# Performance work log

Measured on AMD Instinct MI355X. Metric: run time of the kernel, lower is better.

## Reference

```python
import jax, jax.numpy as jnp
import numpy as np

# architecture constants (from __init__)
F = 34          # input frequency bands
K = 7           # rrf_kernel_size
S = 3           # rrf_stride
F_DOWN = (F - K) // S + 1   # 10
C = 64          # hidden_channels
H = F_DOWN * C  # 640
T_MAX = 9       # max_delay (dilated kernel size of Dcls1d)
PAD = (T_MAX - 1) // 2
MS_KS = 200     # minisobel (freq-dependent high-pass exponential) kernel size
W_MS = 0.75
BN_EPS = 1e-5


def setup_inputs() -> dict:
    key = jax.random.key(0)
    ks = jax.random.split(key, 10)
    B, T = 32, 1000
    def g(k, sh, scale):
        return jax.random.normal(k, sh, jnp.float32) * scale
    x = jax.random.normal(ks[0], (B, 1, F, T), jnp.float32)
    # minisobel params: per-frequency EMA coefficient a in (0,1), mixing weight w
    a_vals = jax.random.uniform(ks[1], (F,), jnp.float32, 0.05, 0.5)
    w_vals = jnp.full((F,), W_MS, jnp.float32)
    # DCLS params: one weight + one continuous delay position per synapse
    dcls_w = g(ks[2], (H, 2 * K), 1.0 / np.sqrt(2 * K * T_MAX))
    dcls_p = jax.random.uniform(ks[3], (H, 2 * K), jnp.float32, 0.0, T_MAX - 1.0)
    dcls_b = jnp.zeros((H,), jnp.float32)
    bn_gamma = jnp.ones((C,), jnp.float32)
    bn_beta = jnp.zeros((C,), jnp.float32)
    s = 1.0 / np.sqrt(H)
    W_ih = g(ks[4], (3 * H, H), s)
    W_hh = g(ks[5], (3 * H, H), s)
    b_ih = g(ks[6], (3 * H,), s)
    b_hh = g(ks[7], (3 * H,), s)
    fc_w = g(ks[8], (1, H), s)
    fc_b = jnp.zeros((1,), jnp.float32)
    return dict(x=x, a_vals=a_vals, w_vals=w_vals, dcls_w=dcls_w, dcls_p=dcls_p,
                dcls_b=dcls_b, bn_gamma=bn_gamma, bn_beta=bn_beta,
                W_ih=W_ih, W_hh=W_hh, b_ih=b_ih, b_hh=b_hh, fc_w=fc_w, fc_b=fc_b)


def reference(x, a_vals, w_vals, dcls_w, dcls_p, dcls_b, bn_gamma, bn_beta,
              W_ih, W_hh, b_ih, b_hh, fc_w, fc_b):
    B, T = x.shape[0], x.shape[-1]
    xf = x[:, 0]  # [B,F,T]

    # --- minisobel: per-frequency causal exponential low-pass, high-pass residual,
    #     on/off rectified channels -> [B,2,F,T]
    t_idx = jnp.arange(MS_KS, dtype=x.dtype)
    ema = a_vals[:, None] * (1.0 - a_vals[:, None]) ** t_idx[None, :]  # [F,200]
    ema = ema[:, ::-1][:, None, :]  # flip so correlation = causal convolution
    low = jax.lax.conv_general_dilated(xf, ema, (1,), [(MS_KS - 1, 0)],
                                       dimension_numbers=('NCH', 'OIH', 'NCH'),
                                       feature_group_count=F)
    hp = xf - w_vals[None, :, None] * low
    x2 = jnp.stack([jax.nn.relu(hp), jax.nn.relu(-hp)], axis=1)  # [B,2,F,T]

    # --- unfold over frequency (kernel (K,T), stride (S,1)) + reshape
    #     -> [B, F_down*2*K, T], channels grouped per output frequency band
    rows = jnp.arange(F_DOWN)[:, None] * S + jnp.arange(K)[None, :]  # [F_down,K]
    u = x2[:, :, rows, :]                      # [B,2,F_down,K,T]
    u = u.transpose(0, 2, 1, 3, 4).reshape(B, F_DOWN * 2 * K, T)

    # --- Dcls1d: build interpolated kernel (triangle interpolation of one weight
    #     at a learnable fractional delay), grouped 'same' conv over time
    p = jnp.clip(dcls_p, 0.0, T_MAX - 1.0)     # [H,2K]
    tt = jnp.arange(T_MAX, dtype=x.dtype)
    dk = dcls_w[:, :, None] * jax.nn.relu(1.0 - jnp.abs(tt[None, None, :] - p[:, :, None]))  # [H,2K,T_max]
    y = jax.lax.conv_general_dilated(u, dk, (1,), [(PAD, PAD)],
                                     dimension_numbers=('NCH', 'OIH', 'NCH'),
                                     feature_group_count=F_DOWN)
    y = y + dcls_b[None, :, None]              # [B,H,T]

    # --- [T,B,C,F_down], BatchNorm1d(C) over (T*B, F_down), sigmoid
    y = y.reshape(B, F_DOWN, C, T).transpose(3, 0, 2, 1)  # [T,B,C,F_down]
    mean = y.mean(axis=(0, 1, 3), keepdims=True)
    var = y.var(axis=(0, 1, 3), keepdims=True)
    y = (y - mean) * jax.lax.rsqrt(var + BN_EPS)
    y = jax.nn.sigmoid(y * bn_gamma[None, None, :, None] + 0 + bn_beta[None, None, :, None]) if False else jax.nn.sigmoid(y * bn_gamma[None, None, :, None] + bn_beta[None, None, :, None])

    # --- GRU (torch gate order r,z,n), batch_first output of all hidden states
    seq = y.reshape(T, B, H)
    x_proj = seq @ W_ih.T + b_ih               # [T,B,3H]

    def step(h, xp):
        gh = h @ W_hh.T + b_hh
        xr, xz, xn = jnp.split(xp, 3, axis=-1)
        hr, hz, hn = jnp.split(gh, 3, axis=-1)
        r = jax.nn.sigmoid(xr + hr)
        z = jax.nn.sigmoid(xz + hz)
        n = jnp.tanh(xn + r * hn)
        h = (1.0 - z) * n + z * h
        return h, h

    h0 = jnp.zeros((B, H), x.dtype)
    _, hs = jax.lax.scan(step, h0, x_proj)     # [T,B,H]

    out = hs @ fc_w.T + fc_b                   # [T,B,1]
    return out[..., 0].T                       # [B,T]
```

## Files before the change

### kernel.cpp

```cpp
#include <hip/hip_runtime.h>
#include <hip/hip_fp16.h>
#include <cstdint>

typedef float f4 __attribute__((ext_vector_type(4)));
typedef _Float16 h2v __attribute__((ext_vector_type(2)));
typedef _Float16 half8 __attribute__((ext_vector_type(8)));
typedef unsigned long long u64;


__global__ void k_dk(const float* __restrict__ dcls_w, const float* __restrict__ dcls_p,
                     float* __restrict__ dk) {
    int idx = blockIdx.x * 256 + threadIdx.x;
    if (idx >= 640 * 126) return;
    int h = idx / 126;
    int r = idx % 126;
    int i = r / 9;
    int tau = r % 9;
    float p = dcls_p[h * 14 + i];
    p = fminf(fmaxf(p, 0.f), 8.f);
    float tri = fmaxf(1.f - fabsf((float)tau - p), 0.f);
    dk[idx] = dcls_w[h * 14 + i] * tri;
}

__global__ void k_ema(const float* __restrict__ x, const float* __restrict__ a_vals,
                      const float* __restrict__ w_vals, float* __restrict__ hp) {
    __shared__ float xr[1024];
    int bf = blockIdx.x;
    int f = bf % 34;
    int tid = threadIdx.x;
    const float* xs = x + (size_t)bf * 1000;
    for (int i = tid; i < 1000; i += 256) xr[i] = xs[i];
    for (int i = 1000 + tid; i < 1024; i += 256) xr[i] = 0.f;
    __syncthreads();
    float a = a_vals[f], wv = w_vals[f];
    float om = 1.f - a;
    int t1 = tid, t2 = tid + 256, t3 = tid + 512, t4 = tid + 768;
    bool v4 = (t4 < 1000);
    float a0 = 0.f, a1 = 0.f, a2 = 0.f, a3 = 0.f;
    float coef = a;
    for (int k = 0; k < 200; ++k) {
        a0 += (k <= t1 ? xr[t1 - k] : 0.f) * coef;
        a1 += xr[t2 - k] * coef;
        a2 += xr[t3 - k] * coef;
        a3 += (v4 ? xr[t4 - k] : 0.f) * coef;
        coef *= om;
    }
    float* op = hp + (size_t)bf * 1000;
    op[t1] = xr[t1] - wv * a0;
    op[t2] = xr[t2] - wv * a1;
    op[t3] = xr[t3] - wv * a2;
    if (v4) op[t4] = xr[t4] - wv * a3;
}

__global__ void __launch_bounds__(256) k_conv(const float* __restrict__ hp,
                                              const float* __restrict__ dk,
                                              const float* __restrict__ dcls_b,
                                              float* __restrict__ ybcgt) {
    __shared__ float u[2 * 7 * 264];
    __shared__ float dks[64 * 126];
    int tid = threadIdx.x;
    int t0 = blockIdx.x * 256;
    int g = blockIdx.y;
    int b = blockIdx.z;
    for (int idx = tid; idx < 8064; idx += 256) dks[idx] = dk[g * 8064 + idx];
    for (int idx = tid; idx < 3696; idx += 256) {
        int pm = idx / 1848;
        int rem = idx % 1848;
        int kk = rem / 264;
        int tt = rem % 264;
        int tg = t0 - 4 + tt;
        float v = (tg >= 0 && tg < 1000) ? hp[((size_t)(b * 34 + g * 3 + kk)) * 1000 + tg] : 0.f;
        u[idx] = pm ? fmaxf(-v, 0.f) : fmaxf(v, 0.f);
    }
    __syncthreads();
    int tl = tid & 63;
    int cg4 = tid >> 6;
    float acc[16][4];
#pragma unroll
    for (int ci = 0; ci < 16; ++ci)
#pragma unroll
        for (int tq = 0; tq < 4; ++tq) acc[ci][tq] = 0.f;

    for (int i = 0; i < 14; ++i) {
#pragma unroll
        for (int tau = 0; tau < 9; ++tau) {
            const float* ub = u + i * 264 + tl + tau;
            float u0 = ub[0];
            float u1 = ub[64];
            float u2 = ub[128];
            float u3 = ub[192];
            const float* dp = dks + cg4 * 16 * 126 + i * 9 + tau;
#pragma unroll
            for (int ci = 0; ci < 16; ++ci) {
                float dv = dp[ci * 126];
                acc[ci][0] += u0 * dv;
                acc[ci][1] += u1 * dv;
                acc[ci][2] += u2 * dv;
                acc[ci][3] += u3 * dv;
            }
        }
    }
#pragma unroll
    for (int ci = 0; ci < 16; ++ci) {
        int c = cg4 * 16 + ci;
        float bias = dcls_b[g * 64 + c];
        size_t base = ((size_t)(b * 640 + c * 10 + g)) * 1000;
#pragma unroll
        for (int tq = 0; tq < 4; ++tq) {
            int t = t0 + tq * 64 + tl;
            if (t < 1000) ybcgt[base + t] = acc[ci][tq] + bias;
        }
    }
}

__global__ void k_bnstat(const float* __restrict__ ybcgt, float* __restrict__ bnsum) {
    int c = blockIdx.x / 10;
    int g = blockIdx.x % 10;
    int tid = threadIdx.x;
    float s = 0.f, q = 0.f;
    const float* base = ybcgt + ((size_t)(c * 10 + g)) * 1000;
    for (int b = 0; b < 32; ++b) {
        const float* p = base + (size_t)b * 640000;
        for (int t = tid; t < 1000; t += 256) {
            float v = p[t];
            s += v;
            q += v * v;
        }
    }
    for (int off = 1; off < 64; off <<= 1) {
        s += __shfl_xor(s, off);
        q += __shfl_xor(q, off);
    }
    __shared__ float rs[4], rq[4];
    if ((tid & 63) == 0) { rs[tid >> 6] = s; rq[tid >> 6] = q; }
    __syncthreads();
    if (tid == 0) {
        s = rs[0] + rs[1] + rs[2] + rs[3];
        q = rq[0] + rq[1] + rq[2] + rq[3];
        atomicAdd(&bnsum[c], s);
        atomicAdd(&bnsum[64 + c], q);
    }
}

__global__ void k_bnfin(const float* __restrict__ bnsum, const float* __restrict__ gamma,
                        const float* __restrict__ beta, float* __restrict__ bnp) {
    int c = threadIdx.x;
    const float inv_n = 1.f / 320000.f;
    float mean = bnsum[c] * inv_n;
    float var = bnsum[64 + c] * inv_n - mean * mean;
    float sc = gamma[c] * rsqrtf(var + 1e-5f);
    bnp[c] = sc;
    bnp[64 + c] = beta[c] - mean * sc;
}

__global__ void k_tr(const float* __restrict__ ybcgt, const float* __restrict__ bnp,
                     __half* __restrict__ seq) {
    __shared__ float tile[64 * 65];
    int tid = threadIdx.x;
    int tt0 = blockIdx.x * 64;
    int h0 = blockIdx.y * 64;
    int b = blockIdx.z;
    int tx = tid & 63;
    int ty = tid >> 6;
#pragma unroll
    for (int r = 0; r < 16; ++r) {
        int hh = r * 4 + ty;
        int t = tt0 + tx;
        float v = (t < 1000) ? ybcgt[((size_t)(b * 640 + h0 + hh)) * 1000 + t] : 0.f;
        int c = (h0 + hh) / 10;
        float sarg = bnp[c] * v + bnp[64 + c];
        tile[hh * 65 + tx] = 1.f / (1.f + __expf(-sarg));
    }
    __syncthreads();
#pragma unroll
    for (int r = 0; r < 16; ++r) {
        int t = tt0 + r * 4 + ty;
        if (t < 1000)
            seq[((size_t)t * 32 + b) * 640 + h0 + tx] = __float2half(tile[tx * 65 + r * 4 + ty]);
    }
}

__global__ void __launch_bounds__(256, 2) k_gemm(const __half* __restrict__ A,
                                                 const float* __restrict__ W,
                                                 const float* __restrict__ bih,
                                                 __half* __restrict__ C) {
    __shared__ __align__(16) _Float16 As[128 * 40];
    __shared__ __align__(16) _Float16 Bs[128 * 40];
    const int tid = threadIdx.x;
    const int n0 = blockIdx.x * 128;
    const int m0 = blockIdx.y * 128;
    const int lane = tid & 63;
    const int wid = tid >> 6;
    const int ml = lane & 15;
    const int kq = lane >> 4;
    const int wm = (wid & 1) * 64;
    const int wn = (wid >> 1) * 64;
    const int sr = tid >> 1;
    const int sc = (tid & 1) * 16;

    f4 acc[4][4];
#pragma unroll
    for (int mt = 0; mt < 4; ++mt)
#pragma unroll
        for (int nt = 0; nt < 4; ++nt) acc[mt][nt] = (f4){0.f, 0.f, 0.f, 0.f};

    const __half* Ag = A + (size_t)(m0 + sr) * 640 + sc;
    const float* Wg = W + (size_t)(n0 + sr) * 640 + sc;

    for (int s = 0; s < 20; ++s) {
        const int k0 = s * 32;
        half8 a0 = *(const half8*)(Ag + k0);
        half8 a1 = *(const half8*)(Ag + k0 + 8);
        float4 b0 = *(const float4*)(Wg + k0);
        float4 b1 = *(const float4*)(Wg + k0 + 4);
        float4 b2 = *(const float4*)(Wg + k0 + 8);
        float4 b3 = *(const float4*)(Wg + k0 + 12);
        __syncthreads();
        *(half8*)&As[sr * 40 + sc] = a0;
        *(half8*)&As[sr * 40 + sc + 8] = a1;
        half8 bh0 = {(_Float16)b0.x, (_Float16)b0.y, (_Float16)b0.z, (_Float16)b0.w,
                     (_Float16)b1.x, (_Float16)b1.y, (_Float16)b1.z, (_Float16)b1.w};
        half8 bh1 = {(_Float16)b2.x, (_Float16)b2.y, (_Float16)b2.z, (_Float16)b2.w,
                     (_Float16)b3.x, (_Float16)b3.y, (_Float16)b3.z, (_Float16)b3.w};
        *(half8*)&Bs[sr * 40 + sc] = bh0;
        *(half8*)&Bs[sr * 40 + sc + 8] = bh1;
        __syncthreads();
        half8 af[4], bf[4];
#pragma unroll
        for (int mt = 0; mt < 4; ++mt)
            af[mt] = *(const half8*)&As[(wm + mt * 16 + ml) * 40 + kq * 8];
#pragma unroll
        for (int nt = 0; nt < 4; ++nt)
            bf[nt] = *(const half8*)&Bs[(wn + nt * 16 + ml) * 40 + kq * 8];
#pragma unroll
        for (int mt = 0; mt < 4; ++mt)
#pragma unroll
            for (int nt = 0; nt < 4; ++nt)
                acc[mt][nt] = __builtin_amdgcn_mfma_f32_16x16x32_f16(af[mt], bf[nt],
                                                                     acc[mt][nt], 0, 0, 0);
    }
#pragma unroll
    for (int nt = 0; nt < 4; ++nt) {
        int n = n0 + wn + nt * 16 + ml;
        float bias = bih[n];
#pragma unroll
        for (int mt = 0; mt < 4; ++mt) {
            int mbase = m0 + wm + mt * 16 + kq * 4;
#pragma unroll
            for (int i = 0; i < 4; ++i)
                C[(size_t)(mbase + i) * 1920 + n] = __float2half(acc[mt][nt][i] + bias);
        }
    }
}

__global__ void __launch_bounds__(512, 1) k_gru(const __half* __restrict__ xp,
                                                const float* __restrict__ Whh,
                                                const float* __restrict__ bhh,
                                                const float* __restrict__ fcw,
                                                u64* __restrict__ slowb,
                                                u64* __restrict__ fastb,
                                                float* __restrict__ fcpart) {
    __shared__ __align__(16) h2v h_lds[16 * 324];
    __shared__ __align__(16) float red[4 * 33 * 4];
    __shared__ float fcred[2][4];

    const int tid = threadIdx.x;
    const int blk = blockIdx.x;
    const int grp = blk & 7;
    const int sl = blk >> 3;
    const int lane = tid & 63;
    const int wid = tid >> 6;

    u64* const sbase = slowb + (size_t)grp * 2560;
    u64* const fbase = fastb + (size_t)grp * 2560;

    const int gte = wid >> 1, jt = wid & 1;
    half8 afrag[20];
    if (wid < 6) {
        int m = lane & 15;
        int kq = lane >> 4;
        const float* wrow = Whh + (size_t)(gte * 640 + sl * 32 + jt * 16 + m) * 640;
#pragma unroll
        for (int s = 0; s < 20; ++s) {
            float4 w0 = *(const float4*)&wrow[s * 32 + kq * 8];
            float4 w1 = *(const float4*)&wrow[s * 32 + kq * 8 + 4];
            afrag[s] = (half8){(_Float16)w0.x, (_Float16)w0.y, (_Float16)w0.z, (_Float16)w0.w,
                               (_Float16)w1.x, (_Float16)w1.y, (_Float16)w1.z, (_Float16)w1.w};
        }
    }
    for (int i = tid; i < 16 * 324; i += 512) h_lds[i] = (h2v){(_Float16)0.f, (_Float16)0.f};

    const int e0 = tid, e1 = tid + 512;
    const bool has3 = (tid < 256);
    const int e2 = has3 ? tid + 1024 : tid;

    const int je = tid >> 2;
    const int be = tid & 3;
    float bh_r = 0.f, bh_z = 0.f, bh_n = 0.f, fw = 0.f, hold = 0.f;
    float xr = 0.f, xz = 0.f, xn = 0.f;
    if (tid < 128) {
        int jg = sl * 32 + je;
        bh_r = bhh[jg];
        bh_z = bhh[640 + jg];
        bh_n = bhh[1280 + jg];
        fw = fcw[jg];
        int bg = grp * 4 + be;
        const __half* xpt = xp + (size_t)bg * 1920;
        xr = __half2float(xpt[jg]);
        xz = __half2float(xpt[640 + jg]);
        xn = __half2float(xpt[1280 + jg]);
    }
    __syncthreads();

    for (int t = 0; t < 1000; ++t) {
        u64* const scur = sbase + (size_t)(t & 1) * 1280;
        u64* const snxt = sbase + (size_t)((t + 1) & 1) * 1280;
        u64* const fcur = fbase + (size_t)(t & 1) * 1280;
        u64* const fnxt = fbase + (size_t)((t + 1) & 1) * 1280;

        u64 v0 = 0, v1 = 0, v2 = 0;
        bool g0 = false, g1 = false, g2 = !has3;
        const unsigned tg = (unsigned)t;
        int round = 0;
        for (;;) {
            u64 f0, f1, f2;
            asm volatile(
                "global_load_dwordx2 %0, %3, off sc0\n\t"
                "global_load_dwordx2 %1, %4, off sc0\n\t"
                "global_load_dwordx2 %2, %5, off sc0\n\t"
                "s_waitcnt vmcnt(0)"
                : "=&v"(f0), "=&v"(f1), "=&v"(f2)
                : "v"(fcur + e0), "v"(fcur + e1), "v"(fcur + e2)
                : "memory");
            if (!g0 && (unsigned)(f0 >> 32) == tg) { v0 = f0; g0 = true; }
            if (!g1 && (unsigned)(f1 >> 32) == tg) { v1 = f1; g1 = true; }
            if (!g2 && (unsigned)(f2 >> 32) == tg) { v2 = f2; g2 = true; }
            if (g0 & g1 & g2) break;
            if ((round & 3) == 2) {
                if (!g0) {
                    u64 s0 = __hip_atomic_load(&scur[e0], __ATOMIC_RELAXED, __HIP_MEMORY_SCOPE_AGENT);
                    if ((unsigned)(s0 >> 32) == tg) { v0 = s0; g0 = true; }
                }
                if (!g1) {
                    u64 s1 = __hip_atomic_load(&scur[e1], __ATOMIC_RELAXED, __HIP_MEMORY_SCOPE_AGENT);
                    if ((unsigned)(s1 >> 32) == tg) { v1 = s1; g1 = true; }
                }
                if (!g2) {
                    u64 s2 = __hip_atomic_load(&scur[e2], __ATOMIC_RELAXED, __HIP_MEMORY_SCOPE_AGENT);
                    if ((unsigned)(s2 >> 32) == tg) { v2 = s2; g2 = true; }
                }
                if (g0 & g1 & g2) break;
            }
            __builtin_amdgcn_s_sleep(1);
            ++round;
        }
        {
            union { unsigned u; h2v h; } pk;
            pk.u = (unsigned)v0; h_lds[(e0 & 3) * 324 + (e0 >> 2)] = pk.h;
            pk.u = (unsigned)v1; h_lds[(e1 & 3) * 324 + (e1 >> 2)] = pk.h;
            if (has3) { pk.u = (unsigned)v2; h_lds[(e2 & 3) * 324 + (e2 >> 2)] = pk.h; }
        }
        __syncthreads();

        float nxr = 0.f, nxz = 0.f, nxn = 0.f;
        if (t + 1 < 1000 && tid < 128) {
            int jg = sl * 32 + je;
            int bg = grp * 4 + be;
            const __half* xpt = xp + ((size_t)(t + 1) * 32 + bg) * 1920;
            nxr = __half2float(xpt[jg]);
            nxz = __half2float(xpt[640 + jg]);
            nxn = __half2float(xpt[1280 + jg]);
        }

        if (wid < 6) {
            int bb = lane & 15;
            int kq = lane >> 4;
            const h2v* hb = &h_lds[bb * 324 + kq * 4];
            f4 acc = {0.f, 0.f, 0.f, 0.f};
#pragma unroll
            for (int s = 0; s < 20; ++s) {
                half8 bfrag = *(const half8*)&hb[s * 16];
                acc = __builtin_amdgcn_mfma_f32_16x16x32_f16(afrag[s], bfrag, acc, 0, 0, 0);
            }
            if (bb < 4) {
#pragma unroll
                for (int i = 0; i < 4; ++i)
                    red[(bb * 33 + jt * 16 + kq * 4 + i) * 4 + gte] = acc[i];
            }
        }
        __syncthreads();

        if (tid < 128) {
            f4 rv = *(const f4*)&red[(be * 33 + je) * 4];
            float hr = bh_r + rv.x;
            float hz = bh_z + rv.y;
            float hn = bh_n + rv.z;
            float r_ = 1.f / (1.f + __expf(-(xr + hr)));
            float z_ = 1.f / (1.f + __expf(-(xz + hz)));
            float pre = xn + r_ * hn;
            float e2v = __expf(-2.f * fabsf(pre));
            float tn = (1.f - e2v) / (1.f + e2v);
            float n_ = (pre >= 0.f) ? tn : -tn;
            float hnew = (1.f - z_) * n_ + z_ * hold;
            hold = hnew;
            float hpair = __shfl_xor(hnew, 4);
            if ((je & 1) == 0) {
                union { h2v h2; unsigned u; } cv;
                cv.h2.x = (_Float16)hnew;
                cv.h2.y = (_Float16)hpair;
                u64 val = (u64)cv.u | ((u64)(unsigned)(t + 1) << 32);
                size_t eo = (size_t)((sl * 16 + (je >> 1)) * 4 + be);
                u64* fp = fnxt + eo;
                asm volatile("global_store_dwordx2 %0, %1, off sc0" :: "v"(fp), "v"(val) : "memory");
                (void)__hip_atomic_exchange(snxt + eo, val,
                                            __ATOMIC_RELAXED, __HIP_MEMORY_SCOPE_AGENT);
            }
            float fv = hnew * fw;
            fv += __shfl_xor(fv, 4);
            fv += __shfl_xor(fv, 8);
            fv += __shfl_xor(fv, 16);
            fv += __shfl_xor(fv, 32);
            if (lane < 4) fcred[wid][lane] = fv;
        }
        xr = nxr; xz = nxz; xn = nxn;
        __syncthreads();
        if (tid < 4)
            fcpart[(size_t)blk * 4000 + t * 4 + tid] = fcred[0][tid] + fcred[1][tid];
    }
}

__global__ void k_fc(const float* __restrict__ fcpart, const float* __restrict__ fcb,
                     float* __restrict__ out) {
    int gid = blockIdx.x * 256 + threadIdx.x;
    int t = gid >> 5;
    int b = gid & 31;
    int g = b >> 2, bi = b & 3;
    float s = fcb[0];
    for (int sl = 0; sl < 20; ++sl)
        s += fcpart[(size_t)(g + 8 * sl) * 4000 + t * 4 + bi];
    out[(size_t)b * 1000 + t] = s;
}

extern "C" void kernel_launch(void* const* d_in, const int* in_sizes, int n_in,
                              void* d_out, int out_size, void* d_ws, size_t ws_size,
                              hipStream_t stream) {
    const float* x      = (const float*)d_in[0];
    const float* a_vals = (const float*)d_in[1];
    const float* w_vals = (const float*)d_in[2];
    const float* dcls_w = (const float*)d_in[3];
    const float* dcls_p = (const float*)d_in[4];
    const float* dcls_b = (const float*)d_in[5];
    const float* gamma  = (const float*)d_in[6];
    const float* beta   = (const float*)d_in[7];
    const float* W_ih   = (const float*)d_in[8];
    const float* W_hh   = (const float*)d_in[9];
    const float* b_ih   = (const float*)d_in[10];
    const float* b_hh   = (const float*)d_in[11];
    const float* fc_w   = (const float*)d_in[12];
    const float* fc_b   = (const float*)d_in[13];
    char* w = (char*)d_ws;

    __half* xpH    = (__half*)(w);
    float* ybcgt   = (float*)(w);
    __half* seqH   = (__half*)(w + 122880000);
    float* hp      = (float*)(w + 122880000);
    float* dk      = (float*)(w + 122880000 + 4352000);
    float* fcpart  = (float*)(w + 122880000);
    u64* fastb     = (u64*)(w + 125440000);
    u64* slowb     = (u64*)(w + 163840000);
    float* bnsum   = (float*)(w + 164003840);

    hipMemsetAsync(w + 163840000, 0, 166912, stream);

    k_dk<<<dim3(315), dim3(256), 0, stream>>>(dcls_w, dcls_p, dk);
    k_ema<<<dim3(1088), dim3(256), 0, stream>>>(x, a_vals, w_vals, hp);
    k_conv<<<dim3(4, 10, 32), dim3(256), 0, stream>>>(hp, dk, dcls_b, ybcgt);
    k_bnstat<<<dim3(640), dim3(256), 0, stream>>>(ybcgt, bnsum);
    k_bnfin<<<dim3(1), dim3(64), 0, stream>>>(bnsum, gamma, beta, (float*)(w + 164004352));
    k_tr<<<dim3(16, 10, 32), dim3(256), 0, stream>>>(ybcgt, (float*)(w + 164004352), seqH);
    k_gemm<<<dim3(15, 250), dim3(256), 0, stream>>>(seqH, W_ih, b_ih, xpH);

    hipMemsetAsync(w + 125440000, 0, 163840, stream);

    {
        const __half* xp_a = xpH;
        void* args[] = {(void*)&xp_a, (void*)&W_hh, (void*)&b_hh, (void*)&fc_w,
                        (void*)&slowb, (void*)&fastb, (void*)&fcpart};
        hipLaunchCooperativeKernel((void*)k_gru, dim3(160), dim3(512), args, 0, stream);
    }

    k_fc<<<dim3(125), dim3(256), 0, stream>>>(fcpart, fc_b, (float*)d_out);
}
```

Measured before the change: 3.451 ms.

## Offload GRU hidden-state polling to non-gate waves, lighten barriers, split MFMA chains

The cross-block hidden-state gather now runs only on threads 128-511, so the two gate waves no longer spin on global flags and stay free for the gate math. Each spinning thread now covers up to four entries instead of three. Two __syncthreads are replaced with a raw lgkmcnt wait plus s_barrier, which skips waiting on outstanding vector-memory ops such as the next-step xp prefetch. The 20-step MFMA dependency chain is split into four independent accumulators to hide MFMA latency, at the cost of a slightly different fp32 summation order.

```diff
diff --git a/kernel.cpp b/kernel.cpp
--- a/kernel.cpp
+++ b/kernel.cpp
@@ -260,6 +260,7 @@
                                                 u64* __restrict__ slowb,
                                                 u64* __restrict__ fastb,
                                                 float* __restrict__ fcpart) {
+#define LBAR() asm volatile("s_waitcnt lgkmcnt(0)\n\ts_barrier" ::: "memory")
     __shared__ __align__(16) h2v h_lds[16 * 324];
     __shared__ __align__(16) float red[4 * 33 * 4];
     __shared__ float fcred[2][4];
@@ -290,9 +291,13 @@
     }
     for (int i = tid; i < 16 * 324; i += 512) h_lds[i] = (h2v){(_Float16)0.f, (_Float16)0.f};
 
-    const int e0 = tid, e1 = tid + 512;
-    const bool has3 = (tid < 256);
-    const int e2 = has3 ? tid + 1024 : tid;
+    const int tp = tid - 128;
+    const bool spinner = (tid >= 128);
+    const int E0 = spinner ? tp : 0;
+    const int E1 = spinner ? tp + 384 : 0;
+    const int E2 = spinner ? tp + 768 : 0;
+    const bool has4 = (tp >= 256) && spinner;
+    const int E3 = has4 ? (1152 + (tp - 256)) : 0;
 
     const int je = tid >> 2;
     const int be = tid & 3;
@@ -318,49 +323,71 @@
         u64* const fcur = fbase + (size_t)(t & 1) * 1280;
         u64* const fnxt = fbase + (size_t)((t + 1) & 1) * 1280;
 
-        u64 v0 = 0, v1 = 0, v2 = 0;
-        bool g0 = false, g1 = false, g2 = !has3;
-        const unsigned tg = (unsigned)t;
-        int round = 0;
-        for (;;) {
-            u64 f0, f1, f2;
-            asm volatile(
-                "global_load_dwordx2 %0, %3, off sc0\n\t"
-                "global_load_dwordx2 %1, %4, off sc0\n\t"
-                "global_load_dwordx2 %2, %5, off sc0\n\t"
-                "s_waitcnt vmcnt(0)"
-                : "=&v"(f0), "=&v"(f1), "=&v"(f2)
-                : "v"(fcur + e0), "v"(fcur + e1), "v"(fcur + e2)
-                : "memory");
-            if (!g0 && (unsigned)(f0 >> 32) == tg) { v0 = f0; g0 = true; }
-            if (!g1 && (unsigned)(f1 >> 32) == tg) { v1 = f1; g1 = true; }
-            if (!g2 && (unsigned)(f2 >> 32) == tg) { v2 = f2; g2 = true; }
-            if (g0 & g1 & g2) break;
-            if ((round & 3) == 2) {
-                if (!g0) {
-                    u64 s0 = __hip_atomic_load(&scur[e0], __ATOMIC_RELAXED, __HIP_MEMORY_SCOPE_AGENT);
-                    if ((unsigned)(s0 >> 32) == tg) { v0 = s0; g0 = true; }
+        if (spinner) {
+            u64 v0 = 0, v1 = 0, v2 = 0, v3 = 0;
+            bool g0 = false, g1 = false, g2 = false, g3 = !has4;
+            const unsigned tg = (unsigned)t;
+            int round = 0;
+            for (;;) {
+                if (!has4) {
+                    u64 f0, f1, f2;
+                    asm volatile(
+                        "global_load_dwordx2 %0, %3, off sc0\n\t"
+                        "global_load_dwordx2 %1, %4, off sc0\n\t"
+                        "global_load_dwordx2 %2, %5, off sc0\n\t"
+                        "s_waitcnt vmcnt(0)"
+                        : "=&v"(f0), "=&v"(f1), "=&v"(f2)
+                        : "v"(fcur + E0), "v"(fcur + E1), "v"(fcur + E2)
+                        : "memory");
+                    if (!g0 && (unsigned)(f0 >> 32) == tg) { v0 = f0; g0 = true; }
+                    if (!g1 && (unsigned)(f1 >> 32) == tg) { v1 = f1; g1 = true; }
+                    if (!g2 && (unsigned)(f2 >> 32) == tg) { v2 = f2; g2 = true; }
+                } else {
+                    u64 f0, f1, f2, f3;
+                    asm volatile(
+                        "global_load_dwordx2 %0, %4, off sc0\n\t"
+                        "global_load_dwordx2 %1, %5, off sc0\n\t"
+                        "global_load_dwordx2 %2, %6, off sc0\n\t"
+                        "global_load_dwordx2 %3, %7, off sc0\n\t"
+                        "s_waitcnt vmcnt(0)"
+                        : "=&v"(f0), "=&v"(f1), "=&v"(f2), "=&v"(f3)
+                        : "v"(fcur + E0), "v"(fcur + E1), "v"(fcur + E2), "v"(fcur + E3)
+                        : "memory");
+                    if (!g0 && (unsigned)(f0 >> 32) == tg) { v0 = f0; g0 = true; }
+                    if (!g1 && (unsigned)(f1 >> 32) == tg) { v1 = f1; g1 = true; }
+                    if (!g2 && (unsigned)(f2 >> 32) == tg) { v2 = f2; g2 = true; }
+                    if (!g3 && (unsigned)(f3 >> 32) == tg) { v3 = f3; g3 = true; }
                 }
-                if (!g1) {
-                    u64 s1 = __hip_atomic_load(&scur[e1], __ATOMIC_RELAXED, __HIP_MEMORY_SCOPE_AGENT);
-                    if ((unsigned)(s1 >> 32) == tg) { v1 = s1; g1 = true; }
+                if (g0 & g1 & g2 & g3) break;
+                if ((round & 3) == 2) {
+                    if (!g0) {
+                        u64 s0 = __hip_atomic_load(&scur[E0], __ATOMIC_RELAXED, __HIP_MEMORY_SCOPE_AGENT);
+                        if ((unsigned)(s0 >> 32) == tg) { v0 = s0; g0 = true; }
+                    }
+                    if (!g1) {
+                        u64 s1 = __hip_atomic_load(&scur[E1], __ATOMIC_RELAXED, __HIP_MEMORY_SCOPE_AGENT);
+                        if ((unsigned)(s1 >> 32) == tg) { v1 = s1; g1 = true; }
+                    }
+                    if (!g2) {
+                        u64 s2 = __hip_atomic_load(&scur[E2], __ATOMIC_RELAXED, __HIP_MEMORY_SCOPE_AGENT);
+                        if ((unsigned)(s2 >> 32) == tg) { v2 = s2; g2 = true; }
+                    }
+                    if (!g3) {
+                        u64 s3 = __hip_atomic_load(&scur[E3], __ATOMIC_RELAXED, __HIP_MEMORY_SCOPE_AGENT);
+                        if ((unsigned)(s3 >> 32) == tg) { v3 = s3; g3 = true; }
+                    }
+                    if (g0 & g1 & g2 & g3) break;
                 }
-                if (!g2) {
-                    u64 s2 = __hip_atomic_load(&scur[e2], __ATOMIC_RELAXED, __HIP_MEMORY_SCOPE_AGENT);
-                    if ((unsigned)(s2 >> 32) == tg) { v2 = s2; g2 = true; }
-                }
-                if (g0 & g1 & g2) break;
+                __builtin_amdgcn_s_sleep(1);
+                ++round;
             }
-            __builtin_amdgcn_s_sleep(1);
-            ++round;
-        }
-        {
             union { unsigned u; h2v h; } pk;
-            pk.u = (unsigned)v0; h_lds[(e0 & 3) * 324 + (e0 >> 2)] = pk.h;
-            pk.u = (unsigned)v1; h_lds[(e1 & 3) * 324 + (e1 >> 2)] = pk.h;
-            if (has3) { pk.u = (unsigned)v2; h_lds[(e2 & 3) * 324 + (e2 >> 2)] = pk.h; }
-        }
-        __syncthreads();
+            pk.u = (unsigned)v0; h_lds[(E0 & 3) * 324 + (E0 >> 2)] = pk.h;
+            pk.u = (unsigned)v1; h_lds[(E1 & 3) * 324 + (E1 >> 2)] = pk.h;
+            pk.u = (unsigned)v2; h_lds[(E2 & 3) * 324 + (E2 >> 2)] = pk.h;
+            if (has4) { pk.u = (unsigned)v3; h_lds[(E3 & 3) * 324 + (E3 >> 2)] = pk.h; }
+        }
+        LBAR();
 
         float nxr = 0.f, nxz = 0.f, nxn = 0.f;
         if (t + 1 < 1000 && tid < 128) {
@@ -376,12 +403,20 @@
             int bb = lane & 15;
             int kq = lane >> 4;
             const h2v* hb = &h_lds[bb * 324 + kq * 4];
-            f4 acc = {0.f, 0.f, 0.f, 0.f};
-#pragma unroll
-            for (int s = 0; s < 20; ++s) {
-                half8 bfrag = *(const half8*)&hb[s * 16];
-                acc = __builtin_amdgcn_mfma_f32_16x16x32_f16(afrag[s], bfrag, acc, 0, 0, 0);
+            f4 a0 = {0.f, 0.f, 0.f, 0.f}, a1 = {0.f, 0.f, 0.f, 0.f};
+            f4 a2 = {0.f, 0.f, 0.f, 0.f}, a3 = {0.f, 0.f, 0.f, 0.f};
+#pragma unroll
+            for (int s = 0; s < 20; s += 4) {
+                half8 b0 = *(const half8*)&hb[s * 16];
+                half8 b1 = *(const half8*)&hb[(s + 1) * 16];
+                half8 b2 = *(const half8*)&hb[(s + 2) * 16];
+                half8 b3 = *(const half8*)&hb[(s + 3) * 16];
+                a0 = __builtin_amdgcn_mfma_f32_16x16x32_f16(afrag[s], b0, a0, 0, 0, 0);
+                a1 = __builtin_amdgcn_mfma_f32_16x16x32_f16(afrag[s + 1], b1, a1, 0, 0, 0);
+                a2 = __builtin_amdgcn_mfma_f32_16x16x32_f16(afrag[s + 2], b2, a2, 0, 0, 0);
+                a3 = __builtin_amdgcn_mfma_f32_16x16x32_f16(afrag[s + 3], b3, a3, 0, 0, 0);
             }
+            f4 acc = (a0 + a1) + (a2 + a3);
             if (bb < 4) {
 #pragma unroll
                 for (int i = 0; i < 4; ++i)
@@ -423,10 +458,11 @@
             if (lane < 4) fcred[wid][lane] = fv;
         }
         xr = nxr; xz = nxz; xn = nxn;
-        __syncthreads();
+        LBAR();
         if (tid < 4)
             fcpart[(size_t)blk * 4000 + t * 4 + tid] = fcred[0][tid] + fcred[1][tid];
     }
+#undef LBAR
 }
 
 __global__ void k_fc(const float* __restrict__ fcpart, const float* __restrict__ fcb,
```

Result: no change. 3.460 ms (+0.3%).

## Fuse input projection GEMM into persistent GRU kernel with prefetched sequence tiles

Applied to the files above, without the earlier changes.

Removes the separate W_ih GEMM kernel and its large fp16 xp intermediate. Each GRU block now keeps its slice of W_ih in registers as MFMA fragments and computes the next timestep's input projection in the same step as the recurrent matmul. Sequence rows are prefetched two steps ahead by spare threads into double-buffered LDS. This drops the GEMM launch and the xp write and read traffic, at the cost of more registers, more LDS and extra MFMA work inside the latency-critical recurrent loop.

```diff
diff --git a/kernel.cpp b/kernel.cpp
--- a/kernel.cpp
+++ b/kernel.cpp
@@ -180,88 +180,19 @@
     }
 }
 
-__global__ void __launch_bounds__(256, 2) k_gemm(const __half* __restrict__ A,
-                                                 const float* __restrict__ W,
-                                                 const float* __restrict__ bih,
-                                                 __half* __restrict__ C) {
-    __shared__ __align__(16) _Float16 As[128 * 40];
-    __shared__ __align__(16) _Float16 Bs[128 * 40];
-    const int tid = threadIdx.x;
-    const int n0 = blockIdx.x * 128;
-    const int m0 = blockIdx.y * 128;
-    const int lane = tid & 63;
-    const int wid = tid >> 6;
-    const int ml = lane & 15;
-    const int kq = lane >> 4;
-    const int wm = (wid & 1) * 64;
-    const int wn = (wid >> 1) * 64;
-    const int sr = tid >> 1;
-    const int sc = (tid & 1) * 16;
-
-    f4 acc[4][4];
-#pragma unroll
-    for (int mt = 0; mt < 4; ++mt)
-#pragma unroll
-        for (int nt = 0; nt < 4; ++nt) acc[mt][nt] = (f4){0.f, 0.f, 0.f, 0.f};
-
-    const __half* Ag = A + (size_t)(m0 + sr) * 640 + sc;
-    const float* Wg = W + (size_t)(n0 + sr) * 640 + sc;
-
-    for (int s = 0; s < 20; ++s) {
-        const int k0 = s * 32;
-        half8 a0 = *(const half8*)(Ag + k0);
-        half8 a1 = *(const half8*)(Ag + k0 + 8);
-        float4 b0 = *(const float4*)(Wg + k0);
-        float4 b1 = *(const float4*)(Wg + k0 + 4);
-        float4 b2 = *(const float4*)(Wg + k0 + 8);
-        float4 b3 = *(const float4*)(Wg + k0 + 12);
-        __syncthreads();
-        *(half8*)&As[sr * 40 + sc] = a0;
-        *(half8*)&As[sr * 40 + sc + 8] = a1;
-        half8 bh0 = {(_Float16)b0.x, (_Float16)b0.y, (_Float16)b0.z, (_Float16)b0.w,
-                     (_Float16)b1.x, (_Float16)b1.y, (_Float16)b1.z, (_Float16)b1.w};
-        half8 bh1 = {(_Float16)b2.x, (_Float16)b2.y, (_Float16)b2.z, (_Float16)b2.w,
-                     (_Float16)b3.x, (_Float16)b3.y, (_Float16)b3.z, (_Float16)b3.w};
-        *(half8*)&Bs[sr * 40 + sc] = bh0;
-        *(half8*)&Bs[sr * 40 + sc + 8] = bh1;
-        __syncthreads();
-        half8 af[4], bf[4];
-#pragma unroll
-        for (int mt = 0; mt < 4; ++mt)
-            af[mt] = *(const half8*)&As[(wm + mt * 16 + ml) * 40 + kq * 8];
-#pragma unroll
-        for (int nt = 0; nt < 4; ++nt)
-            bf[nt] = *(const half8*)&Bs[(wn + nt * 16 + ml) * 40 + kq * 8];
-#pragma unroll
-        for (int mt = 0; mt < 4; ++mt)
-#pragma unroll
-            for (int nt = 0; nt < 4; ++nt)
-                acc[mt][nt] = __builtin_amdgcn_mfma_f32_16x16x32_f16(af[mt], bf[nt],
-                                                                     acc[mt][nt], 0, 0, 0);
-    }
-#pragma unroll
-    for (int nt = 0; nt < 4; ++nt) {
-        int n = n0 + wn + nt * 16 + ml;
-        float bias = bih[n];
-#pragma unroll
-        for (int mt = 0; mt < 4; ++mt) {
-            int mbase = m0 + wm + mt * 16 + kq * 4;
-#pragma unroll
-            for (int i = 0; i < 4; ++i)
-                C[(size_t)(mbase + i) * 1920 + n] = __float2half(acc[mt][nt][i] + bias);
-        }
-    }
-}
-
-__global__ void __launch_bounds__(512, 1) k_gru(const __half* __restrict__ xp,
+__global__ void __launch_bounds__(512, 1) k_gru(const __half* __restrict__ seqH,
                                                 const float* __restrict__ Whh,
+                                                const float* __restrict__ Wih,
                                                 const float* __restrict__ bhh,
+                                                const float* __restrict__ bih,
                                                 const float* __restrict__ fcw,
                                                 u64* __restrict__ slowb,
                                                 u64* __restrict__ fastb,
                                                 float* __restrict__ fcpart) {
     __shared__ __align__(16) h2v h_lds[16 * 324];
+    __shared__ __align__(16) h2v s_lds[2 * 16 * 324];
     __shared__ __align__(16) float red[4 * 33 * 4];
+    __shared__ __align__(16) float xpr[2][4 * 97];
     __shared__ float fcred[2][4];
 
     const int tid = threadIdx.x;
@@ -273,42 +204,78 @@
 
     u64* const sbase = slowb + (size_t)grp * 2560;
     u64* const fbase = fastb + (size_t)grp * 2560;
+    const unsigned* const seqU = (const unsigned*)seqH;
 
     const int gte = wid >> 1, jt = wid & 1;
-    half8 afrag[20];
+    half8 afrag[20], xfrag[20];
     if (wid < 6) {
         int m = lane & 15;
         int kq = lane >> 4;
         const float* wrow = Whh + (size_t)(gte * 640 + sl * 32 + jt * 16 + m) * 640;
+        int xrr = 16 * wid + m;
+        const float* xwrow = Wih + (size_t)((xrr >> 5) * 640 + sl * 32 + (xrr & 31)) * 640;
 #pragma unroll
         for (int s = 0; s < 20; ++s) {
             float4 w0 = *(const float4*)&wrow[s * 32 + kq * 8];
             float4 w1 = *(const float4*)&wrow[s * 32 + kq * 8 + 4];
             afrag[s] = (half8){(_Float16)w0.x, (_Float16)w0.y, (_Float16)w0.z, (_Float16)w0.w,
                                (_Float16)w1.x, (_Float16)w1.y, (_Float16)w1.z, (_Float16)w1.w};
+            float4 x0 = *(const float4*)&xwrow[s * 32 + kq * 8];
+            float4 x1 = *(const float4*)&xwrow[s * 32 + kq * 8 + 4];
+            xfrag[s] = (half8){(_Float16)x0.x, (_Float16)x0.y, (_Float16)x0.z, (_Float16)x0.w,
+                               (_Float16)x1.x, (_Float16)x1.y, (_Float16)x1.z, (_Float16)x1.w};
         }
     }
     for (int i = tid; i < 16 * 324; i += 512) h_lds[i] = (h2v){(_Float16)0.f, (_Float16)0.f};
+    for (int i = tid; i < 2 * 16 * 324; i += 512) s_lds[i] = (h2v){(_Float16)0.f, (_Float16)0.f};
 
     const int e0 = tid, e1 = tid + 512;
     const bool has3 = (tid < 256);
     const int e2 = has3 ? tid + 1024 : tid;
 
+    const int tp2 = tid - 384;
+    const bool sstager = (tid >= 384);
+    const int sb2 = sstager ? (tp2 >> 5) : 0;
+    const int skb = sstager ? ((tp2 & 31) * 10) : 0;
+
     const int je = tid >> 2;
     const int be = tid & 3;
     float bh_r = 0.f, bh_z = 0.f, bh_n = 0.f, fw = 0.f, hold = 0.f;
-    float xr = 0.f, xz = 0.f, xn = 0.f;
+    float xb_r = 0.f, xb_z = 0.f, xb_n = 0.f;
     if (tid < 128) {
         int jg = sl * 32 + je;
         bh_r = bhh[jg];
         bh_z = bhh[640 + jg];
         bh_n = bhh[1280 + jg];
         fw = fcw[jg];
-        int bg = grp * 4 + be;
-        const __half* xpt = xp + (size_t)bg * 1920;
-        xr = __half2float(xpt[jg]);
-        xz = __half2float(xpt[640 + jg]);
-        xn = __half2float(xpt[1280 + jg]);
+        xb_r = bih[jg];
+        xb_z = bih[640 + jg];
+        xb_n = bih[1280 + jg];
+    }
+    __syncthreads();
+
+    for (int idx = tid; idx < 2560; idx += 512) {
+        int par = idx / 1280;
+        int e = idx - par * 1280;
+        int b = e / 320;
+        int kp = e - b * 320;
+        unsigned v = seqU[((size_t)(par * 32) + grp * 4 + b) * 320 + kp];
+        union { unsigned u; h2v h; } pk; pk.u = v;
+        s_lds[par * 5184 + b * 324 + kp] = pk.h;
+    }
+    __syncthreads();
+    if (wid < 6) {
+        int bb = lane & 15, kq = lane >> 4;
+        const h2v* sb = &s_lds[0 * 5184 + bb * 324 + kq * 4];
+        f4 xacc = {0.f, 0.f, 0.f, 0.f};
+#pragma unroll
+        for (int s = 0; s < 20; ++s)
+            xacc = __builtin_amdgcn_mfma_f32_16x16x32_f16(xfrag[s], *(const half8*)&sb[s * 16],
+                                                          xacc, 0, 0, 0);
+        if (bb < 4) {
+#pragma unroll
+            for (int i = 0; i < 4; ++i) xpr[0][bb * 97 + wid * 16 + kq * 4 + i] = xacc[i];
+        }
     }
     __syncthreads();
 
@@ -317,6 +284,14 @@
         u64* const snxt = sbase + (size_t)((t + 1) & 1) * 1280;
         u64* const fcur = fbase + (size_t)(t & 1) * 1280;
         u64* const fnxt = fbase + (size_t)((t + 1) & 1) * 1280;
+
+        unsigned sq[10];
+        const bool sload = sstager && (t + 2 < 1000);
+        if (sload) {
+            const unsigned* srow = seqU + ((size_t)(t + 2) * 32 + grp * 4 + sb2) * 320 + skb;
+#pragma unroll
+            for (int i = 0; i < 10; ++i) sq[i] = srow[i];
+        }
 
         u64 v0 = 0, v1 = 0, v2 = 0;
         bool g0 = false, g1 = false, g2 = !has3;
@@ -362,14 +337,13 @@
         }
         __syncthreads();
 
-        float nxr = 0.f, nxz = 0.f, nxn = 0.f;
-        if (t + 1 < 1000 && tid < 128) {
-            int jg = sl * 32 + je;
-            int bg = grp * 4 + be;
-            const __half* xpt = xp + ((size_t)(t + 1) * 32 + bg) * 1920;
-            nxr = __half2float(xpt[jg]);
-            nxz = __half2float(xpt[640 + jg]);
-            nxn = __half2float(xpt[1280 + jg]);
+        if (sload) {
+            union { unsigned u; h2v h; } pk;
+#pragma unroll
+            for (int i = 0; i < 10; ++i) {
+                pk.u = sq[i];
+                s_lds[(t & 1) * 5184 + sb2 * 324 + skb + i] = pk.h;
+            }
         }
 
         if (wid < 6) {
@@ -387,11 +361,28 @@
                 for (int i = 0; i < 4; ++i)
                     red[(bb * 33 + jt * 16 + kq * 4 + i) * 4 + gte] = acc[i];
             }
+            if (t + 1 < 1000) {
+                const h2v* sb = &s_lds[((t + 1) & 1) * 5184 + bb * 324 + kq * 4];
+                f4 xacc = {0.f, 0.f, 0.f, 0.f};
+#pragma unroll
+                for (int s = 0; s < 20; ++s)
+                    xacc = __builtin_amdgcn_mfma_f32_16x16x32_f16(xfrag[s],
+                                                                  *(const half8*)&sb[s * 16],
+                                                                  xacc, 0, 0, 0);
+                if (bb < 4) {
+#pragma unroll
+                    for (int i = 0; i < 4; ++i)
+                        xpr[(t + 1) & 1][bb * 97 + wid * 16 + kq * 4 + i] = xacc[i];
+                }
+            }
         }
         __syncthreads();
 
         if (tid < 128) {
             f4 rv = *(const f4*)&red[(be * 33 + je) * 4];
+            float xr = xpr[t & 1][be * 97 + je] + xb_r;
+            float xz = xpr[t & 1][be * 97 + 32 + je] + xb_z;
+            float xn = xpr[t & 1][be * 97 + 64 + je] + xb_n;
             float hr = bh_r + rv.x;
             float hz = bh_z + rv.y;
             float hn = bh_n + rv.z;
@@ -422,7 +413,6 @@
             fv += __shfl_xor(fv, 32);
             if (lane < 4) fcred[wid][lane] = fv;
         }
-        xr = nxr; xz = nxz; xn = nxn;
         __syncthreads();
         if (tid < 4)
             fcpart[(size_t)blk * 4000 + t * 4 + tid] = fcred[0][tid] + fcred[1][tid];
@@ -460,17 +450,16 @@
     const float* fc_b   = (const float*)d_in[13];
     char* w = (char*)d_ws;
 
-    __half* xpH    = (__half*)(w);
     float* ybcgt   = (float*)(w);
+    float* fcpart  = (float*)(w);
+    u64* fastb     = (u64*)(w + 8000000);
     __half* seqH   = (__half*)(w + 122880000);
     float* hp      = (float*)(w + 122880000);
     float* dk      = (float*)(w + 122880000 + 4352000);
-    float* fcpart  = (float*)(w + 122880000);
-    u64* fastb     = (u64*)(w + 125440000);
     u64* slowb     = (u64*)(w + 163840000);
     float* bnsum   = (float*)(w + 164003840);
 
-    hipMemsetAsync(w + 163840000, 0, 166912, stream);
+    hipMemsetAsync(w + 163840000, 0, 164864, stream);
 
     k_dk<<<dim3(315), dim3(256), 0, stream>>>(dcls_w, dcls_p, dk);
     k_ema<<<dim3(1088), dim3(256), 0, stream>>>(x, a_vals, w_vals, hp);
@@ -478,14 +467,14 @@
     k_bnstat<<<dim3(640), dim3(256), 0, stream>>>(ybcgt, bnsum);
     k_bnfin<<<dim3(1), dim3(64), 0, stream>>>(bnsum, gamma, beta, (float*)(w + 164004352));
     k_tr<<<dim3(16, 10, 32), dim3(256), 0, stream>>>(ybcgt, (float*)(w + 164004352), seqH);
-    k_gemm<<<dim3(15, 250), dim3(256), 0, stream>>>(seqH, W_ih, b_ih, xpH);
-
-    hipMemsetAsync(w + 125440000, 0, 163840, stream);
+
+    hipMemsetAsync(w + 8000000, 0, 163840, stream);
 
     {
-        const __half* xp_a = xpH;
-        void* args[] = {(void*)&xp_a, (void*)&W_hh, (void*)&b_hh, (void*)&fc_w,
-                        (void*)&slowb, (void*)&fastb, (void*)&fcpart};
+        const __half* seq_a = seqH;
+        void* args[] = {(void*)&seq_a, (void*)&W_hh, (void*)&W_ih, (void*)&b_hh,
+                        (void*)&b_ih, (void*)&fc_w, (void*)&slowb, (void*)&fastb,
+                        (void*)&fcpart};
         hipLaunchCooperativeKernel((void*)k_gru, dim3(160), dim3(512), args, 0, stream);
     }
 
```

After: 3.545 ms. +2.7%, slower.
